# Kernel tuning notes

Hardware: AMD Instinct MI355X
Metric: run time of the kernel (lower is better)

Reference implementation:

```python
import jax, jax.numpy as jnp
import numpy as np

B, N, IN_F, E, H, A = 8, 1024, 1024, 256, 4, 64
ALPHA = 0.2          # leaky relu slope
NEG = -9e15          # mask value from original code


def setup_inputs() -> dict:
    key = jax.random.key(0)
    k = jax.random.split(key, 7)
    x = jax.random.normal(k[0], (B * N, IN_F), dtype=jnp.float32)
    adj = jax.random.randint(k[1], (B, N, N), 0, 2, dtype=jnp.int32)
    # per-head GAT params: W (H, IN_F, E); a split into a1, a2 (H, E) each,
    # since cat([Wh_i, Wh_j]) @ a == Wh_i @ a1 + Wh_j @ a2 exactly.
    W = jax.random.normal(k[2], (H, IN_F, E), dtype=jnp.float32) * 0.05
    a1 = jax.random.normal(k[3], (H, E), dtype=jnp.float32) * 0.05
    a2 = jax.random.normal(k[4], (H, E), dtype=jnp.float32) * 0.05
    W_act = jax.random.normal(k[5], (H * E, A), dtype=jnp.float32) * 0.05
    b_act = jnp.zeros((A,), dtype=jnp.float32)
    return {"x": x, "adj": adj, "W": W, "a1": a1, "a2": a2,
            "W_act": W_act, "b_act": b_act}


def reference(x, adj, W, a1, a2, W_act, b_act):
    b, n, _ = adj.shape
    xr = x.reshape(b, n, -1)                                   # (B, N, IN_F)
    Wh = jnp.einsum('bni,hio->hbno', xr, W)                    # (H, B, N, E)
    f1 = jnp.einsum('hbno,ho->hbn', Wh, a1)                    # a . Wh_i part
    f2 = jnp.einsum('hbno,ho->hbn', Wh, a2)                    # a . Wh_j part
    e = jax.nn.leaky_relu(f1[..., :, None] + f2[..., None, :], ALPHA)  # (H,B,N,N)
    e = jnp.where(adj[None] > 0, e, NEG)
    att = jax.nn.softmax(e, axis=-1)                           # masked softmax
    h_prime = jnp.einsum('hbnm,hbmo->hbno', att, Wh)           # (H, B, N, E)
    h_prime = jax.nn.elu(h_prime)                              # concat=True -> elu
    feat = jnp.transpose(h_prime, (1, 2, 0, 3)).reshape(b * n, H * E)
    return feat @ W_act + b_act                                # (B*N, A)
```

## Files before the change

### kernel.cpp

```cpp
#include <hip/hip_runtime.h>
#include <stdint.h>

typedef __attribute__((ext_vector_type(8))) short short8;
typedef __attribute__((ext_vector_type(4))) float f32x4;


__device__ __forceinline__ float b2f(unsigned short u) {
    union { unsigned int i; float f; } v; v.i = ((unsigned int)u) << 16; return v.f;
}
__device__ __forceinline__ unsigned short f2b(float f) {
    union { float f; unsigned int i; } v; v.f = f;
    unsigned int u = v.i;
    u = (u + 0x7FFFu + ((u >> 16) & 1u)) >> 16;
    return (unsigned short)u;
}
__device__ __forceinline__ void glds16(const void* g, const void* l) {
    __builtin_amdgcn_global_load_lds(
        (const __attribute__((address_space(1))) unsigned int*)g,
        (__attribute__((address_space(3))) unsigned int*)l, 16, 0, 0);
}

__device__ __forceinline__ void cvt8(const void* in, unsigned short* out,
                                     int f, int grp) {
    if (f) {
        ((ushort4*)out)[grp * 2]     = ((const ushort4*)in)[grp * 2];
        ((ushort4*)out)[grp * 2 + 1] = ((const ushort4*)in)[grp * 2 + 1];
    } else {
        const float4* p = (const float4*)in + (size_t)grp * 2;
        float4 a = p[0], b = p[1];
        ushort4 o0, o1;
        o0.x = f2b(a.x); o0.y = f2b(a.y); o0.z = f2b(a.z); o0.w = f2b(a.w);
        o1.x = f2b(b.x); o1.y = f2b(b.y); o1.z = f2b(b.z); o1.w = f2b(b.w);
        ((ushort4*)out)[grp * 2]     = o0;
        ((ushort4*)out)[grp * 2 + 1] = o1;
    }
}

__global__ void prep_small(const unsigned int* __restrict__ x,
                           const void* __restrict__ a1, const void* __restrict__ a2,
                           const void* __restrict__ bact,
                           unsigned short* __restrict__ a1b,
                           unsigned short* __restrict__ a2b,
                           unsigned short* __restrict__ bactb,
                           int* __restrict__ flag, float4* __restrict__ fz) {
    __shared__ int sflag;
    int tid = threadIdx.x;
    if (blockIdx.x > 0) {
        fz[(blockIdx.x - 1) * 256 + tid] = float4{0.f, 0.f, 0.f, 0.f};
        return;
    }
    if (tid < 64) {
        unsigned int wv = x[tid];
        unsigned int e = (wv >> 7) & 0xFF;
        unsigned long long m = __ballot(e >= 100 && e <= 140);
        if (tid == 0) { sflag = (__popcll(m) >= 48) ? 1 : 0; flag[0] = sflag; }
    }
    __syncthreads();
    int f = sflag;
    if (tid < 128) cvt8(a1, a1b, f, tid);
    else           cvt8(a2, a2b, f, tid - 128);
    if (tid < 8)   cvt8(bact, bactb, f, tid);
}

__global__ void conv8(const void* __restrict__ in, unsigned short* __restrict__ out,
                      const int* __restrict__ flag, int total8) {
    int i = blockIdx.x * 256 + threadIdx.x;
    if (i >= total8) return;
    cvt8(in, out, *flag, i);
}

__global__ __launch_bounds__(256) void t2_all(
        const void* __restrict__ Win, const void* __restrict__ Wactin,
        unsigned short* __restrict__ WT, unsigned short* __restrict__ WactT,
        const int* __restrict__ flag) {
    __shared__ unsigned int tile[64 * 65];
    int z = blockIdx.z;
    const void* in; unsigned short* out; int C, bt;
    if (z < 4) { in = Win; out = WT; C = 256; bt = z; }
    else { if (blockIdx.x != 0) return; in = Wactin; out = WactT; C = 64; bt = 0; }
    int t = threadIdx.x;
    int c0 = blockIdx.x * 64;
    int r0 = blockIdx.y * 64;
    int rl = t >> 2;
    int cc = (t & 3) * 16;
    size_t ibase = ((size_t)bt * 1024 + (r0 + rl)) * C + c0 + cc;
    unsigned short v[16];
    if (*flag) {
        const unsigned short* p = (const unsigned short*)in + ibase;
        short8 a = *(const short8*)p;
        short8 b = *(const short8*)(p + 8);
#pragma unroll
        for (int j = 0; j < 8; j++) { v[j] = (unsigned short)a[j]; v[8 + j] = (unsigned short)b[j]; }
    } else {
        const float* p = (const float*)in + ibase;
#pragma unroll
        for (int j = 0; j < 16; j++) v[j] = f2b(p[j]);
    }
#pragma unroll
    for (int j = 0; j < 16; j++)
        tile[(cc + j) * 65 + rl] = v[j];
    __syncthreads();
    int cl = t >> 2;
    int rch = (t & 3) * 16;
    unsigned short o[16];
#pragma unroll
    for (int j = 0; j < 16; j++)
        o[j] = (unsigned short)tile[cl * 65 + rch + j];
    unsigned short* op = out + ((size_t)bt * C + (c0 + cl)) * 1024 + r0 + rch;
#pragma unroll
    for (int q = 0; q < 4; q++) {
        ushort4 s; s.x = o[q*4]; s.y = o[q*4+1]; s.z = o[q*4+2]; s.w = o[q*4+3];
        ((ushort4*)op)[q] = s;
    }
}

__global__ void pack_adj(const int* __restrict__ adj,
                         unsigned int* __restrict__ maskT) {
    int gid = blockIdx.x * 256 + threadIdx.x;
    int lane = threadIdx.x & 63;
    unsigned long long m = __ballot(adj[gid] > 0);
    if (lane == 0) {
        int lin = gid >> 6;
        int mw = (lin & 15) * 2;
        int bn = lin >> 4;
        int b = bn >> 10, n = bn & 1023;
        maskT[(size_t)(b * 32 + mw) * 1024 + n]     = (unsigned int)m;
        maskT[(size_t)(b * 32 + mw + 1) * 1024 + n] = (unsigned int)(m >> 32);
    }
}

__global__ __launch_bounds__(256) void k1_gemm(
        const unsigned short* __restrict__ x,
        const unsigned short* __restrict__ WT,
        unsigned short* __restrict__ WhF,
        const unsigned short* __restrict__ a1b,
        const unsigned short* __restrict__ a2b,
        float* __restrict__ f1, float* __restrict__ f2) {
    __shared__ unsigned short smA[8 * 512];
    __shared__ unsigned short smB[8 * 512];
    int tid = threadIdx.x;
    int w = tid >> 6, lane = tid & 63;
    int lr = lane & 15, lq = lane >> 4;
    int col0 = blockIdx.x * 128;
    int row0 = blockIdx.y * 128;
    int h = col0 >> 8;
    int e_base = col0 & 255;
    int b = row0 >> 10;
    int m_base = row0 & 1023;
    int wr = w >> 1, wc = w & 1;

    f32x4 acc[4][4] = {};

    for (int k0 = 0; k0 < 1024; k0 += 32) {
        __syncthreads();
#pragma unroll
        for (int s = 0; s < 2; s++) {
            int g = 2 * w + s;
            const unsigned short* srcA =
                x + (size_t)(row0 + g * 16 + lr) * 1024 + k0 + lq * 8;
            glds16(srcA, &smA[g * 512]);
            const unsigned short* srcB =
                WT + (size_t)(h * 256 + e_base + g * 16 + lr) * 1024 + k0 + lq * 8;
            glds16(srcB, &smB[g * 512]);
        }
        __syncthreads();
        short8 af[4], bf[4];
#pragma unroll
        for (int i = 0; i < 4; i++)
            af[i] = *(const short8*)&smA[(wr * 4 + i) * 512 + lane * 8];
#pragma unroll
        for (int j = 0; j < 4; j++)
            bf[j] = *(const short8*)&smB[(wc * 4 + j) * 512 + lane * 8];
#pragma unroll
        for (int i = 0; i < 4; i++)
#pragma unroll
            for (int j = 0; j < 4; j++)
                acc[i][j] = __builtin_amdgcn_mfma_f32_16x16x32_bf16(
                    af[i], bf[j], acc[i][j], 0, 0, 0);
    }

    int hb = h * 8 + b;
#pragma unroll
    for (int i = 0; i < 4; i++) {
        int mg = wr * 4 + i;
        int mt = (m_base >> 5) + (mg >> 1);
        int mhi = ((mg & 1) << 1) | (lq >> 1);
        int mlo = (lq & 1) * 4;
#pragma unroll
        for (int j = 0; j < 4; j++) {
            int e = e_base + (wc * 4 + j) * 16 + lr;
            int et = e >> 4, el = e & 15;
            ushort4 vs;
            vs.x = f2b(acc[i][j][0]);
            vs.y = f2b(acc[i][j][1]);
            vs.z = f2b(acc[i][j][2]);
            vs.w = f2b(acc[i][j][3]);
            size_t idx = ((size_t)(hb * 16 + et) * 32 + mt) * 512
                         + mhi * 128 + el * 8 + mlo;
            *(ushort4*)&WhF[idx] = vs;
        }
    }

    const float LOG2E = 1.44269504f;
    float a1v[4], a2v[4];
#pragma unroll
    for (int j = 0; j < 4; j++) {
        int e = e_base + (wc * 4 + j) * 16 + lr;
        a1v[j] = b2f(a1b[h * 256 + e]);
        a2v[j] = b2f(a2b[h * 256 + e]);
    }
#pragma unroll
    for (int i = 0; i < 4; i++) {
#pragma unroll
        for (int reg = 0; reg < 4; reg++) {
            float s1 = 0.f, s2 = 0.f;
#pragma unroll
            for (int j = 0; j < 4; j++) {
                s1 += acc[i][j][reg] * a1v[j];
                s2 += acc[i][j][reg] * a2v[j];
            }
            s1 += __shfl_xor(s1, 1, 64); s2 += __shfl_xor(s2, 1, 64);
            s1 += __shfl_xor(s1, 2, 64); s2 += __shfl_xor(s2, 2, 64);
            s1 += __shfl_xor(s1, 4, 64); s2 += __shfl_xor(s2, 4, 64);
            s1 += __shfl_xor(s1, 8, 64); s2 += __shfl_xor(s2, 8, 64);
            if (lr == 0) {
                int m = m_base + (wr * 4 + i) * 16 + lq * 4 + reg;
                atomicAdd(&f1[hb * 1024 + m], s1 * LOG2E);
                atomicAdd(&f2[hb * 1024 + m], s2 * LOG2E);
            }
        }
    }
}

__global__ __launch_bounds__(256, 2) void k2_attn(
        const unsigned short* __restrict__ WhF,
        const unsigned int* __restrict__ maskT,
        const float* __restrict__ f1, const float* __restrict__ f2,
        unsigned short* __restrict__ feat) {
    int tid = threadIdx.x;
    int w = tid >> 6, lane = tid & 63;
    int lr = lane & 15, lq = lane >> 4;
    int bid = blockIdx.x;
    int xcd = bid & 7, idx = bid >> 3;
    int hb = xcd + 8 * (idx >> 4);
    int rg = (idx & 15) * 4 + w;
    int n0 = rg * 16;
    int h = hb >> 3, b = hb & 7;
    int row = n0 + lr;
    float f1n = f1[hb * 1024 + row];
    const unsigned short* whb = WhF + (size_t)hb * 16 * 32 * 512 + lane * 8;
    const unsigned int* mrow = maskT + (size_t)b * 32 * 1024 + row;
    const float* f2row = f2 + hb * 1024;

    f32x4 acc[16] = {};
    float den = 0.f;

    for (int mt = 0; mt < 32; mt++) {
        int m0 = mt * 32;
        unsigned int mw = mrow[(size_t)mt * 1024];
        float4 fA = *(const float4*)(f2row + m0 + lq * 8);
        float4 fB = *(const float4*)(f2row + m0 + lq * 8 + 4);
        short8 fr1[8];
#pragma unroll
        for (int et = 0; et < 8; et++)
            fr1[et] = *(const short8*)(whb + (size_t)(et * 32 + mt) * 512);

        float fmv[8] = {fA.x, fA.y, fA.z, fA.w, fB.x, fB.y, fB.z, fB.w};
        unsigned int msh = mw >> (lq * 8);
        union { unsigned int u[4]; short8 v; } af;
#pragma unroll
        for (int pr = 0; pr < 4; pr++) {
            unsigned int ub[2];
#pragma unroll
            for (int q = 0; q < 2; q++) {
                int j = pr * 2 + q;
                float tL = f1n + fmv[j];
                float eL = fmaxf(tL, 0.2f * tL);
                float pv = ((msh >> j) & 1u) ? exp2f(eL) : 0.f;
                union { float f; unsigned int i; } pu; pu.f = pv;
                ub[q] = pu.i & 0xFFFF0000u;
                union { unsigned int i; float f; } tb; tb.i = ub[q];
                den += tb.f;
            }
            af.u[pr] = (ub[0] >> 16) | ub[1];
        }
        short8 fr2[8];
#pragma unroll
        for (int et = 0; et < 8; et++)
            fr2[et] = *(const short8*)(whb + (size_t)((et + 8) * 32 + mt) * 512);

#pragma unroll
        for (int et = 0; et < 8; et++)
            acc[et] = __builtin_amdgcn_mfma_f32_16x16x32_bf16(
                af.v, fr1[et], acc[et], 0, 0, 0);
#pragma unroll
        for (int et = 0; et < 8; et++)
            acc[8 + et] = __builtin_amdgcn_mfma_f32_16x16x32_bf16(
                af.v, fr2[et], acc[8 + et], 0, 0, 0);
    }

    den += __shfl_xor(den, 16, 64);
    den += __shfl_xor(den, 32, 64);

    float rdr[4];
#pragma unroll
    for (int reg = 0; reg < 4; reg++)
        rdr[reg] = 1.0f / __shfl(den, lq * 4 + reg, 64);

#pragma unroll
    for (int et = 0; et < 16; et++) {
        int e = et * 16 + lr;
#pragma unroll
        for (int reg = 0; reg < 4; reg++) {
            float v = acc[et][reg] * rdr[reg];
            float o = v > 0.f ? v : __expf(v) - 1.f;
            feat[(size_t)(b * 1024 + n0 + lq * 4 + reg) * 1024 + h * 256 + e]
                = f2b(o);
        }
    }
}

__global__ __launch_bounds__(256) void k3_out(
        const unsigned short* __restrict__ feat,
        const unsigned short* __restrict__ WactT,
        const unsigned short* __restrict__ bact,
        void* __restrict__ out, const int* __restrict__ flag) {
    __shared__ unsigned short smA[2 * 512];
    __shared__ unsigned short smB[4 * 512];
    int tid = threadIdx.x;
    int w = tid >> 6, lane = tid & 63;
    int lr = lane & 15, lq = lane >> 4;
    int row0 = blockIdx.x * 32;
    int g = w & 1, ch = w >> 1;
    int bf16out = *flag;
    f32x4 acc[2] = {};

    for (int k0 = 0; k0 < 1024; k0 += 32) {
        __syncthreads();
        if (w < 2) {
            const unsigned short* src =
                feat + (size_t)(row0 + w * 16 + lr) * 1024 + k0 + lq * 8;
            glds16(src, &smA[w * 512]);
        } else {
#pragma unroll
            for (int s = 0; s < 2; s++) {
                int t = (w - 2) * 2 + s;
                const unsigned short* src =
                    WactT + (size_t)(t * 16 + lr) * 1024 + k0 + lq * 8;
                glds16(src, &smB[t * 512]);
            }
        }
        __syncthreads();
        short8 af = *(const short8*)&smA[g * 512 + lane * 8];
#pragma unroll
        for (int j = 0; j < 2; j++) {
            short8 bf = *(const short8*)&smB[(ch * 2 + j) * 512 + lane * 8];
            acc[j] = __builtin_amdgcn_mfma_f32_16x16x32_bf16(af, bf, acc[j], 0, 0, 0);
        }
    }
#pragma unroll
    for (int j = 0; j < 2; j++) {
        int col = ch * 32 + j * 16 + lr;
        float bv = b2f(bact[col]);
#pragma unroll
        for (int rr = 0; rr < 4; rr++) {
            int r = row0 + g * 16 + lq * 4 + rr;
            float val = acc[j][rr] + bv;
            if (bf16out) ((unsigned short*)out)[(size_t)r * 64 + col] = f2b(val);
            else         ((float*)out)[(size_t)r * 64 + col] = val;
        }
    }
}

extern "C" void kernel_launch(void* const* d_in, const int* in_sizes, int n_in,
                              void* d_out, int out_size, void* d_ws, size_t ws_size,
                              hipStream_t stream) {
    const void* x    = d_in[0];
    const int*  adj  = (const int*)d_in[1];
    const void* W    = d_in[2];
    const void* a1   = d_in[3];
    const void* a2   = d_in[4];
    const void* Wact = d_in[5];
    const void* bact = d_in[6];

    char* ws = (char*)d_ws;
    unsigned short* WhF   = (unsigned short*)(ws);
    unsigned short* xb    = (unsigned short*)(ws + 16777216);
    unsigned short* feat  = (unsigned short*)(ws + 16777216);
    unsigned short* WT    = (unsigned short*)(ws + 33554432);
    unsigned int*   maskT = (unsigned int*)(ws + 33554432);
    unsigned short* WactT = (unsigned short*)(ws + 35651584);
    float*          f1    = (float*)(ws + 35782656);
    float*          f2    = (float*)(ws + 35913728);
    unsigned short* a1b   = (unsigned short*)(ws + 36044800);
    unsigned short* a2b   = (unsigned short*)(ws + 36046848);
    unsigned short* bactb = (unsigned short*)(ws + 36048896);
    int*            flag  = (int*)(ws + 36049024);
    if (ws_size < (size_t)36049040) return;

    prep_small<<<65, 256, 0, stream>>>((const unsigned int*)x, a1, a2, bact,
                                       a1b, a2b, bactb, flag, (float4*)f1);
    conv8<<<4096, 256, 0, stream>>>(x, xb, flag, 1048576);
    t2_all<<<dim3(4, 16, 5), 256, 0, stream>>>(W, Wact, WT, WactT, flag);
    k1_gemm<<<dim3(8, 64), 256, 0, stream>>>(xb, WT, WhF, a1b, a2b, f1, f2);
    pack_adj<<<32768, 256, 0, stream>>>(adj, maskT);
    k2_attn<<<512, 256, 0, stream>>>(WhF, maskT, f1, f2, feat);
    k3_out<<<256, 256, 0, stream>>>(feat, WactT, bactb, d_out, flag);
}
```

Before: 235.3 us.

## Fuse attention with output projection and merge prep kernels into one launch

```diff
diff --git a/kernel.cpp b/kernel.cpp
--- a/kernel.cpp
+++ b/kernel.cpp
@@ -36,81 +36,110 @@
     }
 }
 
-__global__ void prep_small(const unsigned int* __restrict__ x,
-                           const void* __restrict__ a1, const void* __restrict__ a2,
-                           const void* __restrict__ bact,
-                           unsigned short* __restrict__ a1b,
-                           unsigned short* __restrict__ a2b,
-                           unsigned short* __restrict__ bactb,
-                           int* __restrict__ flag, float4* __restrict__ fz) {
+__global__ __launch_bounds__(256) void prep_all(
+        const unsigned int* __restrict__ x4,
+        const void* __restrict__ x, const void* __restrict__ W,
+        const void* __restrict__ Wact,
+        const void* __restrict__ a1, const void* __restrict__ a2,
+        const void* __restrict__ bact,
+        unsigned short* __restrict__ xb, unsigned short* __restrict__ WT,
+        unsigned short* __restrict__ WactF,
+        unsigned short* __restrict__ a1b, unsigned short* __restrict__ a2b,
+        unsigned short* __restrict__ bactb,
+        int* __restrict__ flag, float4* __restrict__ fz) {
+    __shared__ unsigned int tile[64 * 65];
     __shared__ int sflag;
     int tid = threadIdx.x;
-    if (blockIdx.x > 0) {
-        fz[(blockIdx.x - 1) * 256 + tid] = float4{0.f, 0.f, 0.f, 0.f};
+    int bid = blockIdx.x;
+    if (bid >= 4352 && bid < 4416) {
+        fz[(bid - 4352) * 256 + tid] = float4{0.f, 0.f, 0.f, 0.f};
         return;
     }
     if (tid < 64) {
-        unsigned int wv = x[tid];
+        unsigned int wv = x4[tid];
         unsigned int e = (wv >> 7) & 0xFF;
         unsigned long long m = __ballot(e >= 100 && e <= 140);
-        if (tid == 0) { sflag = (__popcll(m) >= 48) ? 1 : 0; flag[0] = sflag; }
+        if (tid == 0) sflag = (__popcll(m) >= 48) ? 1 : 0;
     }
     __syncthreads();
     int f = sflag;
-    if (tid < 128) cvt8(a1, a1b, f, tid);
-    else           cvt8(a2, a2b, f, tid - 128);
-    if (tid < 8)   cvt8(bact, bactb, f, tid);
-}
-
-__global__ void conv8(const void* __restrict__ in, unsigned short* __restrict__ out,
-                      const int* __restrict__ flag, int total8) {
-    int i = blockIdx.x * 256 + threadIdx.x;
-    if (i >= total8) return;
-    cvt8(in, out, *flag, i);
-}
-
-__global__ __launch_bounds__(256) void t2_all(
-        const void* __restrict__ Win, const void* __restrict__ Wactin,
-        unsigned short* __restrict__ WT, unsigned short* __restrict__ WactT,
-        const int* __restrict__ flag) {
-    __shared__ unsigned int tile[64 * 65];
-    int z = blockIdx.z;
-    const void* in; unsigned short* out; int C, bt;
-    if (z < 4) { in = Win; out = WT; C = 256; bt = z; }
-    else { if (blockIdx.x != 0) return; in = Wactin; out = WactT; C = 64; bt = 0; }
-    int t = threadIdx.x;
-    int c0 = blockIdx.x * 64;
-    int r0 = blockIdx.y * 64;
-    int rl = t >> 2;
-    int cc = (t & 3) * 16;
-    size_t ibase = ((size_t)bt * 1024 + (r0 + rl)) * C + c0 + cc;
-    unsigned short v[16];
-    if (*flag) {
-        const unsigned short* p = (const unsigned short*)in + ibase;
-        short8 a = *(const short8*)p;
-        short8 b = *(const short8*)(p + 8);
-#pragma unroll
-        for (int j = 0; j < 8; j++) { v[j] = (unsigned short)a[j]; v[8 + j] = (unsigned short)b[j]; }
-    } else {
-        const float* p = (const float*)in + ibase;
-#pragma unroll
-        for (int j = 0; j < 16; j++) v[j] = f2b(p[j]);
-    }
-#pragma unroll
-    for (int j = 0; j < 16; j++)
-        tile[(cc + j) * 65 + rl] = v[j];
-    __syncthreads();
-    int cl = t >> 2;
-    int rch = (t & 3) * 16;
-    unsigned short o[16];
-#pragma unroll
-    for (int j = 0; j < 16; j++)
-        o[j] = (unsigned short)tile[cl * 65 + rch + j];
-    unsigned short* op = out + ((size_t)bt * C + (c0 + cl)) * 1024 + r0 + rch;
-#pragma unroll
-    for (int q = 0; q < 4; q++) {
-        ushort4 s; s.x = o[q*4]; s.y = o[q*4+1]; s.z = o[q*4+2]; s.w = o[q*4+3];
-        ((ushort4*)op)[q] = s;
+
+    if (bid < 4096) {
+        cvt8(x, xb, f, bid * 256 + tid);
+        return;
+    }
+    if (bid < 4352) {
+        int lb = bid - 4096;
+        int c0 = (lb & 3) * 64;
+        int r0 = ((lb >> 2) & 15) * 64;
+        int bt = lb >> 6;
+        int rl = tid >> 2;
+        int cc = (tid & 3) * 16;
+        size_t ibase = ((size_t)bt * 1024 + (r0 + rl)) * 256 + c0 + cc;
+        unsigned short v[16];
+        if (f) {
+            const unsigned short* p = (const unsigned short*)W + ibase;
+            short8 a = *(const short8*)p;
+            short8 b = *(const short8*)(p + 8);
+#pragma unroll
+            for (int j = 0; j < 8; j++) { v[j] = (unsigned short)a[j]; v[8 + j] = (unsigned short)b[j]; }
+        } else {
+            const float* p = (const float*)W + ibase;
+#pragma unroll
+            for (int j = 0; j < 16; j++) v[j] = f2b(p[j]);
+        }
+#pragma unroll
+        for (int j = 0; j < 16; j++)
+            tile[(cc + j) * 65 + rl] = v[j];
+        __syncthreads();
+        int cl = tid >> 2;
+        int rch = (tid & 3) * 16;
+        unsigned short o[16];
+#pragma unroll
+        for (int j = 0; j < 16; j++)
+            o[j] = (unsigned short)tile[cl * 65 + rch + j];
+        unsigned short* op = WT + ((size_t)bt * 256 + (c0 + cl)) * 1024 + r0 + rch;
+#pragma unroll
+        for (int q = 0; q < 4; q++) {
+            ushort4 s; s.x = o[q*4]; s.y = o[q*4+1]; s.z = o[q*4+2]; s.w = o[q*4+3];
+            ((ushort4*)op)[q] = s;
+        }
+        return;
+    }
+    if (bid == 4416) {
+        if (tid == 0) flag[0] = f;
+        if (tid < 128) cvt8(a1, a1b, f, tid);
+        else           cvt8(a2, a2b, f, tid - 128);
+        if (tid < 8)   cvt8(bact, bactb, f, tid);
+        return;
+    }
+    {
+        int lb = bid - 4417;
+#pragma unroll
+        for (int ktt = 0; ktt < 2; ktt++) {
+            int kt = lb * 2 + ktt;
+            int kl = tid >> 3;
+            int cg = (tid & 7) * 8;
+            int k = kt * 32 + kl;
+            unsigned short v[8];
+            if (f) {
+                const unsigned short* p = (const unsigned short*)Wact + (size_t)k * 64 + cg;
+                short8 a = *(const short8*)p;
+#pragma unroll
+                for (int j = 0; j < 8; j++) v[j] = (unsigned short)a[j];
+            } else {
+                const float* p = (const float*)Wact + (size_t)k * 64 + cg;
+#pragma unroll
+                for (int j = 0; j < 8; j++) v[j] = f2b(p[j]);
+            }
+#pragma unroll
+            for (int q = 0; q < 8; q++) {
+                int col = cg + q;
+                size_t dst = ((size_t)(kt * 4 + (col >> 4)) * 512)
+                             + (((kl >> 3) & 3) * 16 + (col & 15)) * 8 + (kl & 7);
+                WactF[dst] = v[q];
+            }
+        }
     }
 }
 
@@ -232,20 +261,21 @@
     }
 }
 
-__global__ __launch_bounds__(256, 2) void k2_attn(
+__global__ __launch_bounds__(256, 2) void k2k3(
         const unsigned short* __restrict__ WhF,
         const unsigned int* __restrict__ maskT,
         const float* __restrict__ f1, const float* __restrict__ f2,
-        unsigned short* __restrict__ feat) {
+        const unsigned short* __restrict__ WactF,
+        const unsigned short* __restrict__ bactb,
+        void* __restrict__ out, const int* __restrict__ flag) {
+    __shared__ unsigned short sfeat[32 * 512];
     int tid = threadIdx.x;
     int w = tid >> 6, lane = tid & 63;
     int lr = lane & 15, lq = lane >> 4;
-    int bid = blockIdx.x;
-    int xcd = bid & 7, idx = bid >> 3;
-    int hb = xcd + 8 * (idx >> 4);
-    int rg = (idx & 15) * 4 + w;
-    int n0 = rg * 16;
-    int h = hb >> 3, b = hb & 7;
+    int b = blockIdx.x & 7;
+    int n0 = (blockIdx.x >> 3) * 16;
+    int h = w;
+    int hb = h * 8 + b;
     int row = n0 + lr;
     float f1n = f1[hb * 1024 + row];
     const unsigned short* whb = WhF + (size_t)hb * 16 * 32 * 512 + lane * 8;
@@ -301,7 +331,6 @@
 
     den += __shfl_xor(den, 16, 64);
     den += __shfl_xor(den, 32, 64);
-
     float rdr[4];
 #pragma unroll
     for (int reg = 0; reg < 4; reg++)
@@ -309,66 +338,35 @@
 
 #pragma unroll
     for (int et = 0; et < 16; et++) {
-        int e = et * 16 + lr;
+        int kt = h * 8 + (et >> 1);
+        int sub = (et & 1) * 2 + (lr >> 3);
+        int j = lr & 7;
 #pragma unroll
         for (int reg = 0; reg < 4; reg++) {
+            int r = lq * 4 + reg;
             float v = acc[et][reg] * rdr[reg];
             float o = v > 0.f ? v : __expf(v) - 1.f;
-            feat[(size_t)(b * 1024 + n0 + lq * 4 + reg) * 1024 + h * 256 + e]
-                = f2b(o);
-        }
-    }
-}
-
-__global__ __launch_bounds__(256) void k3_out(
-        const unsigned short* __restrict__ feat,
-        const unsigned short* __restrict__ WactT,
-        const unsigned short* __restrict__ bact,
-        void* __restrict__ out, const int* __restrict__ flag) {
-    __shared__ unsigned short smA[2 * 512];
-    __shared__ unsigned short smB[4 * 512];
-    int tid = threadIdx.x;
-    int w = tid >> 6, lane = tid & 63;
-    int lr = lane & 15, lq = lane >> 4;
-    int row0 = blockIdx.x * 32;
-    int g = w & 1, ch = w >> 1;
+            sfeat[kt * 512 + (sub * 16 + r) * 8 + j] = f2b(o);
+        }
+    }
+    __syncthreads();
+
+    f32x4 oacc = {};
+#pragma unroll 8
+    for (int kt = 0; kt < 32; kt++) {
+        short8 a = *(const short8*)&sfeat[kt * 512 + lane * 8];
+        short8 bf = *(const short8*)&WactF[(size_t)(kt * 4 + w) * 512 + lane * 8];
+        oacc = __builtin_amdgcn_mfma_f32_16x16x32_bf16(a, bf, oacc, 0, 0, 0);
+    }
     int bf16out = *flag;
-    f32x4 acc[2] = {};
-
-    for (int k0 = 0; k0 < 1024; k0 += 32) {
-        __syncthreads();
-        if (w < 2) {
-            const unsigned short* src =
-                feat + (size_t)(row0 + w * 16 + lr) * 1024 + k0 + lq * 8;
-            glds16(src, &smA[w * 512]);
-        } else {
-#pragma unroll
-            for (int s = 0; s < 2; s++) {
-                int t = (w - 2) * 2 + s;
-                const unsigned short* src =
-                    WactT + (size_t)(t * 16 + lr) * 1024 + k0 + lq * 8;
-                glds16(src, &smB[t * 512]);
-            }
-        }
-        __syncthreads();
-        short8 af = *(const short8*)&smA[g * 512 + lane * 8];
-#pragma unroll
-        for (int j = 0; j < 2; j++) {
-            short8 bf = *(const short8*)&smB[(ch * 2 + j) * 512 + lane * 8];
-            acc[j] = __builtin_amdgcn_mfma_f32_16x16x32_bf16(af, bf, acc[j], 0, 0, 0);
-        }
-    }
-#pragma unroll
-    for (int j = 0; j < 2; j++) {
-        int col = ch * 32 + j * 16 + lr;
-        float bv = b2f(bact[col]);
-#pragma unroll
-        for (int rr = 0; rr < 4; rr++) {
-            int r = row0 + g * 16 + lq * 4 + rr;
-            float val = acc[j][rr] + bv;
-            if (bf16out) ((unsigned short*)out)[(size_t)r * 64 + col] = f2b(val);
-            else         ((float*)out)[(size_t)r * 64 + col] = val;
-        }
+    int col = w * 16 + lr;
+    float bv = b2f(bactb[col]);
+#pragma unroll
+    for (int reg = 0; reg < 4; reg++) {
+        int r = b * 1024 + n0 + lq * 4 + reg;
+        float val = oacc[reg] + bv;
+        if (bf16out) ((unsigned short*)out)[(size_t)r * 64 + col] = f2b(val);
+        else         ((float*)out)[(size_t)r * 64 + col] = val;
     }
 }
 
@@ -386,10 +384,9 @@
     char* ws = (char*)d_ws;
     unsigned short* WhF   = (unsigned short*)(ws);
     unsigned short* xb    = (unsigned short*)(ws + 16777216);
-    unsigned short* feat  = (unsigned short*)(ws + 16777216);
     unsigned short* WT    = (unsigned short*)(ws + 33554432);
     unsigned int*   maskT = (unsigned int*)(ws + 33554432);
-    unsigned short* WactT = (unsigned short*)(ws + 35651584);
+    unsigned short* WactF = (unsigned short*)(ws + 35651584);
     float*          f1    = (float*)(ws + 35782656);
     float*          f2    = (float*)(ws + 35913728);
     unsigned short* a1b   = (unsigned short*)(ws + 36044800);
@@ -398,12 +395,10 @@
     int*            flag  = (int*)(ws + 36049024);
     if (ws_size < (size_t)36049040) return;
 
-    prep_small<<<65, 256, 0, stream>>>((const unsigned int*)x, a1, a2, bact,
+    prep_all<<<4433, 256, 0, stream>>>((const unsigned int*)x, x, W, Wact,
+                                       a1, a2, bact, xb, WT, WactF,
                                        a1b, a2b, bactb, flag, (float4*)f1);
-    conv8<<<4096, 256, 0, stream>>>(x, xb, flag, 1048576);
-    t2_all<<<dim3(4, 16, 5), 256, 0, stream>>>(W, Wact, WT, WactT, flag);
     k1_gemm<<<dim3(8, 64), 256, 0, stream>>>(xb, WT, WhF, a1b, a2b, f1, f2);
     pack_adj<<<32768, 256, 0, stream>>>(adj, maskT);
-    k2_attn<<<512, 256, 0, stream>>>(WhF, maskT, f1, f2, feat);
-    k3_out<<<256, 256, 0, stream>>>(feat, WactT, bactb, d_out, flag);
-}
+    k2k3<<<512, 256, 0, stream>>>(WhF, maskT, f1, f2, WactF, bactb, d_out, flag);
+}
```

Measured after the change: 304.7 us. 29.5% more time.
